# Kernel optimization log

Measured on AMD Instinct MI355X. Metric: run time of the kernel, lower is better.

Reference implementation:

```python
import jax, jax.numpy as jnp
import numpy as np
from jax import lax

DG = 8          # deformable groups
KH = KW = 3
K = KH * KW
PAD = 1


def conv3x3(x, w, b):
    # x: (B,C,H,W), w: (O,C,3,3) -> SAME conv, stride 1
    y = lax.conv_general_dilated(x, w, (1, 1), ((PAD, PAD), (PAD, PAD)),
                                 dimension_numbers=('NCHW', 'OIHW', 'NCHW'))
    return y + b[None, :, None, None]


def lrelu(x):
    return jnp.where(x >= 0, x, 0.1 * x)


def modulated_deform_conv(x, offset, mask, w, b):
    """DCNv2 semantics: stride=1, pad=1, dilation=1, groups=1.
    x: (B,C,H,W); offset: (B, 2*DG*K, H, W); mask: (B, DG*K, H, W) (already sigmoided);
    w: (O, C, 3, 3); b: (O,).
    Offset channel layout per CUDA kernel: (DG, K, 2[y,x]).
    """
    B, C, H, W = x.shape
    cg = C // DG
    off = offset.reshape(B, DG, K, 2, H, W)
    dy, dx = off[:, :, :, 0], off[:, :, :, 1]            # (B,DG,K,H,W)

    ky, kx = jnp.meshgrid(jnp.arange(KH), jnp.arange(KW), indexing='ij')
    ky = ky.reshape(K).astype(x.dtype)
    kx = kx.reshape(K).astype(x.dtype)
    base_y = jnp.arange(H, dtype=x.dtype)[None, :, None] - PAD + ky[:, None, None]  # (K,H,1)
    base_x = jnp.arange(W, dtype=x.dtype)[None, None, :] - PAD + kx[:, None, None]  # (K,1,W)
    py = dy + base_y                                     # (B,DG,K,H,W)
    px = dx + base_x

    y0 = jnp.floor(py)
    x0 = jnp.floor(px)
    wy = py - y0
    wx = px - x0
    y0i = y0.astype(jnp.int32)
    x0i = x0.astype(jnp.int32)

    xg = x.reshape(B, DG, cg, H * W)

    def gather(yi, xi):
        valid = ((yi >= 0) & (yi < H) & (xi >= 0) & (xi < W)).astype(x.dtype)
        idx = jnp.clip(yi, 0, H - 1) * W + jnp.clip(xi, 0, W - 1)   # (B,DG,K,H,W)
        idxf = idx.reshape(B, DG, 1, K * H * W)
        vals = jnp.take_along_axis(xg, jnp.broadcast_to(idxf, (B, DG, cg, K * H * W)), axis=3)
        return vals.reshape(B, DG, cg, K, H, W) * valid[:, :, None]

    samp = gather(y0i, x0i) * ((1 - wy) * (1 - wx))[:, :, None]
    samp = samp + gather(y0i, x0i + 1) * ((1 - wy) * wx)[:, :, None]
    samp = samp + gather(y0i + 1, x0i) * (wy * (1 - wx))[:, :, None]
    samp = samp + gather(y0i + 1, x0i + 1) * (wy * wx)[:, :, None]

    samp = samp * mask.reshape(B, DG, 1, K, H, W)        # modulated
    wr = w.reshape(w.shape[0], DG, cg, K)
    out = jnp.einsum('odck,bdckhw->bohw', wr, samp)
    return out + b[None, :, None, None]


def dcn_pack(x, feat, off_w, off_b, w, b):
    # conv_offset on `feat` -> (B, 3*DG*K, H, W); chunk into o1,o2,mask
    out = conv3x3(feat, off_w, off_b)
    o1, o2, m = jnp.split(out, 3, axis=1)
    offset = jnp.concatenate([o1, o2], axis=1)
    mask = jax.nn.sigmoid(m)
    return modulated_deform_conv(x, offset, mask, w, b)


def setup_inputs() -> dict:
    key = jax.random.key(0)
    ks = jax.random.split(key, 24)
    B, C, H, W = 4, 64, 192, 192
    nf = C

    def wconv(k, o, i, s=0.02):
        return jax.random.normal(k, (o, i, 3, 3), jnp.float32) * s

    inp = {
        'nbr_l1': jax.random.normal(ks[0], (B, C, H, W), jnp.float32),
        'ref_l1': jax.random.normal(ks[1], (B, C, H, W), jnp.float32),
        'oc1_w': wconv(ks[2], nf, 2 * nf), 'oc1_b': jnp.zeros((nf,), jnp.float32),
        'oc2_w': wconv(ks[3], nf, nf), 'oc2_b': jnp.zeros((nf,), jnp.float32),
        'dcn1_off_w': wconv(ks[4], 3 * DG * K, nf, 0.01), 'dcn1_off_b': jnp.zeros((3 * DG * K,), jnp.float32),
        'dcn1_w': wconv(ks[5], nf, nf), 'dcn1_b': jnp.zeros((nf,), jnp.float32),
        'fc_w': wconv(ks[6], nf, nf), 'fc_b': jnp.zeros((nf,), jnp.float32),
        'cas1_w': wconv(ks[7], nf, 2 * nf), 'cas1_b': jnp.zeros((nf,), jnp.float32),
        'cas2_w': wconv(ks[8], nf, nf), 'cas2_b': jnp.zeros((nf,), jnp.float32),
        'casd_off_w': wconv(ks[9], 3 * DG * K, nf, 0.01), 'casd_off_b': jnp.zeros((3 * DG * K,), jnp.float32),
        'casd_w': wconv(ks[10], nf, nf), 'casd_b': jnp.zeros((nf,), jnp.float32),
    }
    return inp


def reference(nbr_l1, ref_l1, oc1_w, oc1_b, oc2_w, oc2_b,
              dcn1_off_w, dcn1_off_b, dcn1_w, dcn1_b, fc_w, fc_b,
              cas1_w, cas1_b, cas2_w, cas2_b,
              casd_off_w, casd_off_b, casd_w, casd_b):
    offset = jnp.concatenate([nbr_l1, ref_l1], axis=1)
    offset = lrelu(conv3x3(offset, oc1_w, oc1_b))
    offset = lrelu(conv3x3(offset, oc2_w, oc2_b))
    feat = dcn_pack(nbr_l1, offset, dcn1_off_w, dcn1_off_b, dcn1_w, dcn1_b)
    feat = conv3x3(feat, fc_w, fc_b)                     # no activation (matches source)
    offset = jnp.concatenate([feat, ref_l1], axis=1)
    offset = lrelu(conv3x3(lrelu(conv3x3(offset, cas1_w, cas1_b)), cas2_w, cas2_b))
    feat = lrelu(dcn_pack(feat, offset, casd_off_w, casd_off_b, casd_w, casd_b))
    return feat
```

## Files before the change

kernel.cpp:

```cpp
#include <hip/hip_runtime.h>
#include <hip/hip_bf16.h>
#include <math.h>

typedef __hip_bfloat16 bf16;
typedef float  floatx16 __attribute__((ext_vector_type(16)));
typedef short  short8   __attribute__((ext_vector_type(8)));

#define Bn 4
#define NF 64
#define Hn 192
#define Wn 192
#define HWn (Hn*Wn)

#define WA_OC1  0
#define WA_OC2  73728
#define WA_FC   110592
#define WA_CAS1 147456
#define WA_CAS2 221184
#define WA_D1O  258048
#define WA_CDO  405504
#define WP_D1   552960
#define WP_CD   589824
#define B_OC1  0
#define B_OC2  64
#define B_FC   128
#define B_CAS1 192
#define B_CAS2 256
#define B_D1O  320
#define B_CDO  536
#define B_D1P  752
#define B_CDP  816
#define BIAS_OFF  1024
#define WPOOL_OFF 5120
#define BUF_OFF   1261568
#define FEAT_BYTES 18874368

#define WROWS 12
#define WCOLS 12
#define WSTR  72
#define SSTR2 152

__device__ __forceinline__ float b2f(bf16 v){ return __bfloat162float(v); }
__device__ __forceinline__ bf16  f2b(float v){ return __float2bfloat16(v); }
__device__ __forceinline__ float us2f(unsigned short u){ return __uint_as_float(((unsigned)u) << 16); }
__device__ __forceinline__ float ld(const void* p, size_t i, int f32){
    if (f32) return ((const float*)p)[i];
    return b2f(((const bf16*)p)[i]);
}

union B8 { uint2 u2[2]; uint4 u4; short8 s8; };
union V8 { uint4 u4; unsigned short us[8]; bf16 h[8]; };
union V4 { uint2 u2; bf16 h[4]; };

struct P20 { const void* p[20]; int n[20]; };

__global__ void detect_kernel(P20 a, int* __restrict__ flags){
    int t = threadIdx.x;
    if (t >= 20) return;
    const unsigned short* u = (const unsigned short*)a.p[t];
    int n = a.n[t]; if (n > 512) n = 512;
    int f32 = 0;
    for (int i = 0; i < n; ++i){
        float v = __uint_as_float(((unsigned)u[i]) << 16);
        if (!(fabsf(v) < 1e3f)) f32 = 1;
    }
    flags[t] = f32;
}

__global__ void prep_convA(const void* __restrict__ src, const int* __restrict__ flags,
                           int fi, bf16* __restrict__ dst, int Cin, int CoutReal, int OCB)
{
    int idx = blockIdx.x*256 + threadIdx.x;
    int KK = Cin >> 4;
    int total = OCB*9*KK*512;
    if (idx >= total) return;
    int j  = idx & 7;
    int ko = (idx>>3) & 1;
    int m  = (idx>>4) & 31;
    int rest = idx >> 9;
    int kk = rest % KK; rest /= KK;
    int tap = rest % 9;
    int ocb = rest / 9;
    int oc = ocb*32 + m;
    int ci = kk*16 + ko*8 + j;
    float v = 0.f;
    if (oc < CoutReal) v = ld(src, ((size_t)oc*Cin + ci)*9 + tap, flags[fi]);
    dst[idx] = f2b(v);
}

__global__ void prep_projA(const void* __restrict__ src, const int* __restrict__ flags,
                           int fi, bf16* __restrict__ dst)
{
    int idx = blockIdx.x*256 + threadIdx.x;
    if (idx >= 2*36*512) return;
    int j  = idx & 7;
    int ko = (idx>>3) & 1;
    int m  = (idx>>4) & 31;
    int rest = idx >> 9;
    int kk = rest % 36;
    int ocb = rest / 36;
    int oc = ocb*32 + m;
    int kp   = kk*16 + ko*8 + j;
    int slot = kp >> 3;
    int cg   = kp & 7;
    int dg   = slot / 9;
    int tap  = slot - dg*9;
    int k    = (dg*8 + cg)*9 + tap;
    dst[idx] = f2b(ld(src, (size_t)oc*576 + k, flags[fi]));
}

__global__ void prep_bias(P20 a, const int* __restrict__ flags, float* __restrict__ bp){
    int t = threadIdx.x;
    const int src[9] = {3,5,11,13,15,7,17,9,19};
    const int off[9] = {B_OC1,B_OC2,B_FC,B_CAS1,B_CAS2,B_D1O,B_CDO,B_D1P,B_CDP};
    const int sz[9]  = {64,64,64,64,64,216,216,64,64};
    for (int s = 0; s < 9; ++s)
        if (t < sz[s]) bp[off[s] + t] = ld(a.p[src[s]], t, flags[src[s]]);
}

__global__ __launch_bounds__(256)
void pack_x(const void* __restrict__ src, const int* __restrict__ flags, int fi,
            bf16* __restrict__ dst)
{
    __shared__ bf16 s[64*65];
    const int b    = blockIdx.y;
    const int pix0 = blockIdx.x * 64;
    const int t    = threadIdx.x;
    const int f    = (fi >= 0) ? flags[fi] : 0;

    const int px8 = (t & 7) * 8;
    const int ci0 = t >> 3;
#pragma unroll
    for (int it = 0; it < 2; ++it){
        int ci = ci0 + it*32;
        size_t g = ((size_t)b*NF + ci)*HWn + pix0 + px8;
        if (f){
            float4 a0 = *(const float4*)((const float*)src + g);
            float4 a1 = *(const float4*)((const float*)src + g + 4);
            bf16* sp = &s[ci*65 + px8];
            sp[0]=f2b(a0.x); sp[1]=f2b(a0.y); sp[2]=f2b(a0.z); sp[3]=f2b(a0.w);
            sp[4]=f2b(a1.x); sp[5]=f2b(a1.y); sp[6]=f2b(a1.z); sp[7]=f2b(a1.w);
        } else {
            V8 v; v.u4 = *(const uint4*)((const bf16*)src + g);
            bf16* sp = &s[ci*65 + px8];
#pragma unroll
            for (int j = 0; j < 8; ++j) sp[j] = v.h[j];
        }
    }
    __syncthreads();

    const int px  = t >> 2;
    const int ch0 = (t & 3) * 16;
    V8 o0, o1;
#pragma unroll
    for (int j = 0; j < 8; ++j){
        o0.h[j] = s[(ch0 + j)*65 + px];
        o1.h[j] = s[(ch0 + 8 + j)*65 + px];
    }
    bf16* dp = dst + ((size_t)b*HWn + pix0 + px)*64 + ch0;
    *(uint4*)(dp)     = o0.u4;
    *(uint4*)(dp + 8) = o1.u4;
}

__global__ __launch_bounds__(256)
void conv_mfma(const bf16* __restrict__ inA, const bf16* __restrict__ inB,
               const bf16* __restrict__ wA, const float* __restrict__ bias,
               bf16* __restrict__ out,
               int nOcb, int CoutReal, int OutChStore, int ACT)
{
    extern __shared__ __align__(16) char smem_raw[];
    bf16* s_in = (bf16*)smem_raw;

    const int CinT  = inB ? 128 : 64;
    const int ciPad = CinT + 4;
    const int b     = blockIdx.z;
    const int pix0  = blockIdx.x * 64;
    const int h     = pix0 / Wn;
    const int x0    = pix0 - h*Wn;
    const int tid   = threadIdx.x;

    for (int ky = 0; ky < 3; ++ky){
        const int y  = h - 1 + ky;
        const bool yv = (unsigned)y < (unsigned)Hn;
        const size_t rb = ((size_t)b*HWn + (size_t)y*Wn)*64;
        for (int e = tid; e < 528; e += 256){
            const int c = e >> 3, ch8 = e & 7;
            const int x = x0 - 1 + c;
            const bool v = yv && (unsigned)x < (unsigned)Wn;
            B8 va; va.u4 = make_uint4(0,0,0,0);
            if (v) va.u4 = *(const uint4*)(inA + rb + (size_t)x*64 + ch8*8);
            bf16* dp = &s_in[(ky*66 + c)*ciPad + ch8*8];
            *(uint2*)(dp)     = va.u2[0];
            *(uint2*)(dp + 4) = va.u2[1];
            if (inB){
                B8 vb; vb.u4 = make_uint4(0,0,0,0);
                if (v) vb.u4 = *(const uint4*)(inB + rb + (size_t)x*64 + ch8*8);
                bf16* dq = dp + 64;
                *(uint2*)(dq)     = vb.u2[0];
                *(uint2*)(dq + 4) = vb.u2[1];
            }
        }
    }
    __syncthreads();

    const int w    = tid >> 6;
    const int lane = tid & 63;
    const int m    = lane & 31;
    const int half = lane >> 5;
    const int och  = (w >> 1) * 32;
    const int pxh  = (w & 1) * 32;
    const int KK   = CinT >> 4;
    const int col0 = pxh + m;
    const int pxo  = pix0 + pxh + m;

    for (int ot = 0; ot < nOcb; ++ot){
        const int ocb = ot*2 + (w >> 1);
        floatx16 acc;
#pragma unroll
        for (int r = 0; r < 16; ++r) acc[r] = 0.f;

        const bf16* wAb = wA + ((size_t)ocb*9*KK)*512 + m*16 + half*8;
#pragma unroll
        for (int tap = 0; tap < 9; ++tap){
            const int ky = tap/3, kx = tap - (tap/3)*3;
            const bf16* srow = s_in + (ky*66 + col0 + kx)*ciPad + half*8;
            for (int kk = 0; kk < KK; ++kk){
                B8 ba; ba.u4 = *(const uint4*)(wAb + (size_t)(tap*KK + kk)*512);
                B8 bb;
                const bf16* sp = srow + kk*16;
                bb.u2[0] = *(const uint2*)(sp);
                bb.u2[1] = *(const uint2*)(sp + 4);
                acc = __builtin_amdgcn_mfma_f32_32x32x16_bf16(ba.s8, bb.s8, acc, 0, 0, 0);
            }
        }

        if (ACT == 2){
#pragma unroll
            for (int r = 0; r < 16; ++r){
                int row = (r & 3) + 8*(r >> 2) + 4*half;
                int oc  = ot*64 + och + row;
                if (oc < CoutReal){
                    float v = acc[r] + bias[oc];
                    if (oc >= 144) v = 1.f/(1.f + expf(-v));
                    out[((size_t)b*OutChStore + oc)*HWn + pxo] = f2b(v);
                }
            }
        } else {
            bf16* ob = out + ((size_t)b*HWn + pxo)*64 + och + 4*half;
#pragma unroll
            for (int q = 0; q < 4; ++q){
                V4 u;
#pragma unroll
                for (int j = 0; j < 4; ++j){
                    int oc = och + 4*half + 8*q + j;
                    float v = acc[q*4 + j] + bias[oc];
                    if (ACT == 1) v = (v >= 0.f) ? v : 0.1f*v;
                    u.h[j] = f2b(v);
                }
                *(uint2*)(ob + 8*q) = u.u2;
            }
        }
    }
}

__global__ __launch_bounds__(256, 2)
void dcn_mfma(const bf16* __restrict__ xi,
              const bf16* __restrict__ offs,
              const bf16* __restrict__ wP,
              const float* __restrict__ pbias,
              void* __restrict__ out, int outF32, int ACT)
{
    __shared__ __align__(16) bf16 s_win[WROWS*WCOLS*WSTR];
    __shared__ __align__(16) bf16 s_samp[64*SSTR2];

    const int b   = blockIdx.y;
    const int bx  = blockIdx.x;
    const int tx  = bx % (Wn/8);
    const int ty  = bx / (Wn/8);
    const int gx0 = tx*8, gy0 = ty*8;
    const int wx0 = gx0 - 2, wy0 = gy0 - 2;
    const int tid = threadIdx.x;

    const bf16* xb = xi + (size_t)b*HWn*64;

    for (int c = tid; c < WROWS*WCOLS*8; c += 256){
        int ch4 = c & 7;
        int pxi = c >> 3;
        int gy  = wy0 + pxi/WCOLS;
        int gx  = wx0 + pxi%WCOLS;
        uint4 v = {0u,0u,0u,0u};
        if ((unsigned)gy < (unsigned)Hn && (unsigned)gx < (unsigned)Wn)
            v = *(const uint4*)(xb + ((size_t)gy*Wn + gx)*64 + ch4*8);
        *(uint4*)&s_win[pxi*WSTR + ch4*8] = v;
    }

    const int px   = tid & 63;
    const int wq   = tid >> 6;
    const int pr   = px >> 3, pc = px & 7;
    const int gy   = gy0 + pr, gx = gx0 + pc;
    const int m    = px & 31;
    const int half = px >> 5;
    const int och  = (wq >> 1) * 32;
    const int pxh  = (wq & 1) * 32;

    const size_t obase = (size_t)b*216*HWn + (size_t)gy*Wn + gx;
    const uint4 z4 = {0u,0u,0u,0u};

    const bf16* wPb  = wP + ((size_t)(wq>>1)*36)*512 + m*16 + half*8;
    const bf16* srow = s_samp + (pxh + m)*SSTR2 + half*8;

    floatx16 acc;
#pragma unroll
    for (int r = 0; r < 16; ++r) acc[r] = 0.f;

    for (int pass = 0; pass < 4; ++pass){
        __syncthreads();

#pragma unroll
        for (int ii = 0; ii < 5; ++ii){
            int sl = wq + ii*4;
            if (sl < 18){
                int dgl = sl / 9;
                int tap = sl - dgl*9;
                int dg  = pass*2 + dgl;
                int ky  = tap / 3;
                int kx  = tap - ky*3;
                float dy = b2f(offs[obase + (size_t)(dg*18 + tap*2    )*HWn]);
                float dx = b2f(offs[obase + (size_t)(dg*18 + tap*2 + 1)*HWn]);
                float mk = b2f(offs[obase + (size_t)(144 + dg*9 + tap )*HWn]);
                float py  = dy + (float)(gy - 1 + ky);
                float pxx = dx + (float)(gx - 1 + kx);
                float y0f = floorf(py), x0f = floorf(pxx);
                int   y0  = (int)y0f,   xi0 = (int)x0f;
                float wy  = py - y0f,   wx  = pxx - x0f;
                float w00 = (1.f-wy)*(1.f-wx)*mk, w01 = (1.f-wy)*wx*mk;
                float w10 = wy*(1.f-wx)*mk,       w11 = wy*wx*mk;
                int ly = y0 - wy0, lx = xi0 - wx0;

                auto fetch = [&](int ly_, int lx_, int y_, int x_) -> uint4 {
                    if ((unsigned)ly_ < (unsigned)WROWS && (unsigned)lx_ < (unsigned)WCOLS)
                        return *(const uint4*)&s_win[(ly_*WCOLS + lx_)*WSTR + dg*8];
                    if ((unsigned)y_ < (unsigned)Hn && (unsigned)x_ < (unsigned)Wn)
                        return *(const uint4*)(xb + ((size_t)y_*Wn + x_)*64 + dg*8);
                    return z4;
                };
                V8 c00, c01, c10, c11, o;
                c00.u4 = fetch(ly,   lx,   y0,   xi0  );
                c01.u4 = fetch(ly,   lx+1, y0,   xi0+1);
                c10.u4 = fetch(ly+1, lx,   y0+1, xi0  );
                c11.u4 = fetch(ly+1, lx+1, y0+1, xi0+1);
#pragma unroll
                for (int j = 0; j < 8; ++j){
                    float v = w00*us2f(c00.us[j]) + w01*us2f(c01.us[j])
                            + w10*us2f(c10.us[j]) + w11*us2f(c11.us[j]);
                    o.h[j] = f2b(v);
                }
                *(uint4*)&s_samp[px*SSTR2 + sl*8] = o.u4;
            }
        }
        __syncthreads();

#pragma unroll
        for (int kk = 0; kk < 9; ++kk){
            B8 ba; ba.u4 = *(const uint4*)(wPb + (size_t)(pass*9 + kk)*512);
            B8 bb; bb.u4 = *(const uint4*)(srow + kk*16);
            acc = __builtin_amdgcn_mfma_f32_32x32x16_bf16(ba.s8, bb.s8, acc, 0, 0, 0);
        }
    }

    const int opx = pxh + m;
    const int pxo = (gy0 + (opx >> 3))*Wn + gx0 + (opx & 7);
    if (outF32){
#pragma unroll
        for (int r = 0; r < 16; ++r){
            int row = (r & 3) + 8*(r >> 2) + 4*half;
            int oc  = och + row;
            float v = acc[r] + pbias[oc];
            if (ACT) v = (v >= 0.f) ? v : 0.1f*v;
            ((float*)out)[((size_t)b*NF + oc)*HWn + pxo] = v;
        }
    } else {
        bf16* ob = (bf16*)out + ((size_t)b*HWn + pxo)*64 + och + 4*half;
#pragma unroll
        for (int q = 0; q < 4; ++q){
            V4 u;
#pragma unroll
            for (int j = 0; j < 4; ++j){
                int oc = och + 4*half + 8*q + j;
                float v = acc[q*4 + j] + pbias[oc];
                if (ACT) v = (v >= 0.f) ? v : 0.1f*v;
                u.h[j] = f2b(v);
            }
            *(uint2*)(ob + 8*q) = u.u2;
        }
    }
}

extern "C" void kernel_launch(void* const* d_in, const int* in_sizes, int n_in,
                              void* d_out, int out_size, void* d_ws, size_t ws_size,
                              hipStream_t stream)
{
    enum { I_NBR=0, I_REF=1, I_OC1W=2, I_OC2W=4, I_D1OW=6, I_D1W=8, I_FCW=10,
           I_C1W=12, I_C2W=14, I_CDOW=16, I_CDW=18 };

    int*   flags = (int*)d_ws;
    float* bp    = (float*)((char*)d_ws + BIAS_OFF);
    bf16*  wp    = (bf16*) ((char*)d_ws + WPOOL_OFF);
    bf16*  t1    = (bf16*) ((char*)d_ws + BUF_OFF);
    bf16*  f1    = (bf16*) ((char*)d_ws + BUF_OFF + FEAT_BYTES);
    bf16*  offs  = (bf16*) ((char*)d_ws + BUF_OFF + 2*(size_t)FEAT_BYTES);
    bf16*  t0    = (bf16*) d_out;
    bf16*  nbr_i = (bf16*)((char*)d_out + FEAT_BYTES);
    bf16*  refA  = offs;
    bf16*  refB  = nbr_i;

    P20 a;
    for (int i = 0; i < 20; ++i){ a.p[i] = d_in[i]; a.n[i] = in_sizes[i]; }

    detect_kernel<<<1, 64, 0, stream>>>(a, flags);
    prep_bias<<<1, 256, 0, stream>>>(a, flags, bp);
    prep_convA<<<288, 256, 0, stream>>>(d_in[I_OC1W], flags, I_OC1W, wp+WA_OC1, 128, 64, 2);
    prep_convA<<<144, 256, 0, stream>>>(d_in[I_OC2W], flags, I_OC2W, wp+WA_OC2,  64, 64, 2);
    prep_convA<<<144, 256, 0, stream>>>(d_in[I_FCW],  flags, I_FCW,  wp+WA_FC,   64, 64, 2);
    prep_convA<<<288, 256, 0, stream>>>(d_in[I_C1W],  flags, I_C1W,  wp+WA_CAS1,128, 64, 2);
    prep_convA<<<144, 256, 0, stream>>>(d_in[I_C2W],  flags, I_C2W,  wp+WA_CAS2, 64, 64, 2);
    prep_convA<<<576, 256, 0, stream>>>(d_in[I_D1OW], flags, I_D1OW, wp+WA_D1O,  64, 216, 8);
    prep_convA<<<576, 256, 0, stream>>>(d_in[I_CDOW], flags, I_CDOW, wp+WA_CDO,  64, 216, 8);
    prep_projA<<<144, 256, 0, stream>>>(d_in[I_D1W],  flags, I_D1W,  wp+WP_D1);
    prep_projA<<<144, 256, 0, stream>>>(d_in[I_CDW],  flags, I_CDW,  wp+WP_CD);

    dim3 blk(256,1,1);
    const int smem64  = 3*66*68*2;
    const int smem128 = 3*66*132*2;
    dim3 gC (576, 1, Bn);
    dim3 gD (576, Bn, 1);
    dim3 gP (576, Bn, 1);

    pack_x<<<gP, blk, 0, stream>>>(d_in[I_NBR], flags, I_NBR, nbr_i);
    pack_x<<<gP, blk, 0, stream>>>(d_in[I_REF], flags, I_REF, refA);
    conv_mfma<<<gC, blk, smem128, stream>>>(nbr_i, refA, wp+WA_OC1, bp+B_OC1,
        t0, 1, 64, 64, 1);
    conv_mfma<<<gC, blk, smem64, stream>>>(t0, nullptr, wp+WA_OC2, bp+B_OC2,
        t1, 1, 64, 64, 1);
    conv_mfma<<<gC, blk, smem64, stream>>>(t1, nullptr, wp+WA_D1O, bp+B_D1O,
        offs, 4, 216, 216, 2);
    dcn_mfma<<<gD, blk, 0, stream>>>(nbr_i, offs, wp+WP_D1, bp+B_D1P,
        t1, 0, 0);
    pack_x<<<gP, blk, 0, stream>>>(d_in[I_REF], flags, I_REF, refB);
    conv_mfma<<<gC, blk, smem64, stream>>>(t1, nullptr, wp+WA_FC, bp+B_FC,
        f1, 1, 64, 64, 0);
    conv_mfma<<<gC, blk, smem128, stream>>>(f1, refB, wp+WA_CAS1, bp+B_CAS1,
        t0, 1, 64, 64, 1);
    conv_mfma<<<gC, blk, smem64, stream>>>(t0, nullptr, wp+WA_CAS2, bp+B_CAS2,
        t1, 1, 64, 64, 1);
    conv_mfma<<<gC, blk, smem64, stream>>>(t1, nullptr, wp+WA_CDO, bp+B_CDO,
        offs, 4, 216, 216, 2);
    dcn_mfma<<<gD, blk, 0, stream>>>(f1, offs, wp+WP_CD, bp+B_CDP,
        d_out, 1, 1);
}
```

Baseline: 893.7 us.

## Tile conv over two output rows with double-buffered weights and merged prep kernels

The conv kernel now computes a 2-row by 64-pixel tile per block, with each wave issuing two MFMAs per weight fragment. This halves the weight loads per output and shares the input halo rows. Weight fragments are prefetched through a two-slot register ring, and channel counts become template parameters so the loops are fully unrolled. The weight and bias preparation launches are merged into two kernels to cut launch overhead, at the cost of higher register pressure and more shared memory per block.

```diff
diff --git a/kernel.cpp b/kernel.cpp
--- a/kernel.cpp
+++ b/kernel.cpp
@@ -54,68 +54,69 @@
 
 struct P20 { const void* p[20]; int n[20]; };
 
-__global__ void detect_kernel(P20 a, int* __restrict__ flags){
+__global__ void detect_bias(P20 a, int* __restrict__ flags, float* __restrict__ bp){
+    __shared__ int sf[20];
     int t = threadIdx.x;
-    if (t >= 20) return;
-    const unsigned short* u = (const unsigned short*)a.p[t];
-    int n = a.n[t]; if (n > 512) n = 512;
-    int f32 = 0;
-    for (int i = 0; i < n; ++i){
-        float v = __uint_as_float(((unsigned)u[i]) << 16);
-        if (!(fabsf(v) < 1e3f)) f32 = 1;
-    }
-    flags[t] = f32;
-}
-
-__global__ void prep_convA(const void* __restrict__ src, const int* __restrict__ flags,
-                           int fi, bf16* __restrict__ dst, int Cin, int CoutReal, int OCB)
-{
-    int idx = blockIdx.x*256 + threadIdx.x;
-    int KK = Cin >> 4;
-    int total = OCB*9*KK*512;
-    if (idx >= total) return;
-    int j  = idx & 7;
-    int ko = (idx>>3) & 1;
-    int m  = (idx>>4) & 31;
-    int rest = idx >> 9;
-    int kk = rest % KK; rest /= KK;
-    int tap = rest % 9;
-    int ocb = rest / 9;
-    int oc = ocb*32 + m;
-    int ci = kk*16 + ko*8 + j;
-    float v = 0.f;
-    if (oc < CoutReal) v = ld(src, ((size_t)oc*Cin + ci)*9 + tap, flags[fi]);
-    dst[idx] = f2b(v);
-}
-
-__global__ void prep_projA(const void* __restrict__ src, const int* __restrict__ flags,
-                           int fi, bf16* __restrict__ dst)
-{
-    int idx = blockIdx.x*256 + threadIdx.x;
-    if (idx >= 2*36*512) return;
-    int j  = idx & 7;
-    int ko = (idx>>3) & 1;
-    int m  = (idx>>4) & 31;
-    int rest = idx >> 9;
-    int kk = rest % 36;
-    int ocb = rest / 36;
-    int oc = ocb*32 + m;
-    int kp   = kk*16 + ko*8 + j;
-    int slot = kp >> 3;
-    int cg   = kp & 7;
-    int dg   = slot / 9;
-    int tap  = slot - dg*9;
-    int k    = (dg*8 + cg)*9 + tap;
-    dst[idx] = f2b(ld(src, (size_t)oc*576 + k, flags[fi]));
-}
-
-__global__ void prep_bias(P20 a, const int* __restrict__ flags, float* __restrict__ bp){
-    int t = threadIdx.x;
+    if (t < 20){
+        const unsigned short* u = (const unsigned short*)a.p[t];
+        int n = a.n[t]; if (n > 512) n = 512;
+        int f32 = 0;
+        for (int i = 0; i < n; ++i){
+            float v = __uint_as_float(((unsigned)u[i]) << 16);
+            if (!(fabsf(v) < 1e3f)) f32 = 1;
+        }
+        sf[t] = f32; flags[t] = f32;
+    }
+    __syncthreads();
     const int src[9] = {3,5,11,13,15,7,17,9,19};
     const int off[9] = {B_OC1,B_OC2,B_FC,B_CAS1,B_CAS2,B_D1O,B_CDO,B_D1P,B_CDP};
     const int sz[9]  = {64,64,64,64,64,216,216,64,64};
     for (int s = 0; s < 9; ++s)
-        if (t < sz[s]) bp[off[s] + t] = ld(a.p[src[s]], t, flags[src[s]]);
+        if (t < sz[s]) bp[off[s] + t] = ld(a.p[src[s]], t, sf[src[s]]);
+}
+
+__global__ void prep_weights(P20 a, const int* __restrict__ flags, bf16* __restrict__ wp)
+{
+    const int srcI[9] = {2,4,10,12,14,6,16,8,18};
+    const int dstO[9] = {WA_OC1,WA_OC2,WA_FC,WA_CAS1,WA_CAS2,WA_D1O,WA_CDO,WP_D1,WP_CD};
+    const int cinA[9] = {128,64,64,128,64,64,64,0,0};
+    const int coutA[9]= {64,64,64,64,64,216,216,0,0};
+    const int nblk[9] = {288,144,144,288,144,576,576,144,144};
+
+    int bx = blockIdx.x;
+    int j = 0, base = 0;
+    while (j < 8 && bx >= base + nblk[j]){ base += nblk[j]; ++j; }
+    int idx = (bx - base)*256 + threadIdx.x;
+    const void* src = a.p[srcI[j]];
+    const int f = flags[srcI[j]];
+    bf16* dst = wp + dstO[j];
+
+    int jj = idx & 7;
+    int ko = (idx>>3) & 1;
+    int mm = (idx>>4) & 31;
+    int rest = idx >> 9;
+    if (cinA[j]){
+        int KK = cinA[j] >> 4;
+        int kk = rest % KK; rest /= KK;
+        int tap = rest % 9;
+        int ocb = rest / 9;
+        int oc = ocb*32 + mm;
+        int ci = kk*16 + ko*8 + jj;
+        float v = 0.f;
+        if (oc < coutA[j]) v = ld(src, ((size_t)oc*cinA[j] + ci)*9 + tap, f);
+        dst[idx] = f2b(v);
+    } else {
+        int kk = rest % 36;
+        int ocb = rest / 36;
+        int oc = ocb*32 + mm;
+        int kp   = kk*16 + ko*8 + jj;
+        int slot = kp >> 3;
+        int cg   = kp & 7;
+        int dg   = slot / 9;
+        int tap  = slot - dg*9;
+        int k    = (dg*8 + cg)*9 + tap;
+        dst[idx] = f2b(ld(src, (size_t)oc*576 + k, f));
+    }
 }
 
 __global__ __launch_bounds__(256)
@@ -162,43 +163,41 @@
     *(uint4*)(dp + 8) = o1.u4;
 }
 
-__global__ __launch_bounds__(256)
+template<int KK, int NOCB>
+__global__ __launch_bounds__(256, 2)
 void conv_mfma(const bf16* __restrict__ inA, const bf16* __restrict__ inB,
                const bf16* __restrict__ wA, const float* __restrict__ bias,
-               bf16* __restrict__ out,
-               int nOcb, int CoutReal, int OutChStore, int ACT)
+               bf16* __restrict__ out, int ACT)
 {
+    constexpr int CinT  = KK*16;
+    constexpr int ciPad = CinT + 4;
+    constexpr int CH8   = CinT/8;
+    constexpr int CSH   = (KK==4)?3:4;
     extern __shared__ __align__(16) char smem_raw[];
     bf16* s_in = (bf16*)smem_raw;
 
-    const int CinT  = inB ? 128 : 64;
-    const int ciPad = CinT + 4;
-    const int b     = blockIdx.z;
-    const int pix0  = blockIdx.x * 64;
-    const int h     = pix0 / Wn;
-    const int x0    = pix0 - h*Wn;
-    const int tid   = threadIdx.x;
-
-    for (int ky = 0; ky < 3; ++ky){
-        const int y  = h - 1 + ky;
+    const int b  = blockIdx.z;
+    const int bx = blockIdx.x;
+    const int ty = bx/3, tx = bx - ty*3;
+    const int h0 = ty*2, x0 = tx*64;
+    const int tid = threadIdx.x;
+
+    for (int r = 0; r < 4; ++r){
+        const int y = h0 - 1 + r;
         const bool yv = (unsigned)y < (unsigned)Hn;
         const size_t rb = ((size_t)b*HWn + (size_t)y*Wn)*64;
-        for (int e = tid; e < 528; e += 256){
-            const int c = e >> 3, ch8 = e & 7;
+        for (int e = tid; e < 66*CH8; e += 256){
+            const int c   = e >> CSH;
+            const int ch8 = e & (CH8-1);
             const int x = x0 - 1 + c;
-            const bool v = yv && (unsigned)x < (unsigned)Wn;
-            B8 va; va.u4 = make_uint4(0,0,0,0);
-            if (v) va.u4 = *(const uint4*)(inA + rb + (size_t)x*64 + ch8*8);
-            bf16* dp = &s_in[(ky*66 + c)*ciPad + ch8*8];
-            *(uint2*)(dp)     = va.u2[0];
-            *(uint2*)(dp + 4) = va.u2[1];
-            if (inB){
-                B8 vb; vb.u4 = make_uint4(0,0,0,0);
-                if (v) vb.u4 = *(const uint4*)(inB + rb + (size_t)x*64 + ch8*8);
-                bf16* dq = dp + 64;
-                *(uint2*)(dq)     = vb.u2[0];
-                *(uint2*)(dq + 4) = vb.u2[1];
-            }
+            B8 v; v.u4 = make_uint4(0,0,0,0);
+            if (yv && (unsigned)x < (unsigned)Wn){
+                if (KK==8 && ch8 >= 8) v.u4 = *(const uint4*)(inB + rb + (size_t)x*64 + (ch8-8)*8);
+                else                   v.u4 = *(const uint4*)(inA + rb + (size_t)x*64 + ch8*8);
+            }
+            bf16* dp = &s_in[(size_t)(r*66 + c)*ciPad + ch8*8];
+            *(uint2*)(dp)     = v.u2[0];
+            *(uint2*)(dp + 4) = v.u2[1];
         }
     }
     __syncthreads();
@@ -208,56 +207,80 @@
     const int m    = lane & 31;
     const int half = lane >> 5;
     const int och  = (w >> 1) * 32;
-    const int pxh  = (w & 1) * 32;
-    const int KK   = CinT >> 4;
-    const int col0 = pxh + m;
-    const int pxo  = pix0 + pxh + m;
-
-    for (int ot = 0; ot < nOcb; ++ot){
+    const int rw   = (w & 1);
+    const int gpx0 = (h0 + rw)*Wn + x0;
+
+#pragma unroll
+    for (int ot = 0; ot < NOCB; ++ot){
         const int ocb = ot*2 + (w >> 1);
-        floatx16 acc;
-#pragma unroll
-        for (int r = 0; r < 16; ++r) acc[r] = 0.f;
-
-        const bf16* wAb = wA + ((size_t)ocb*9*KK)*512 + m*16 + half*8;
+        const bf16* wb = wA + ((size_t)ocb*9*KK)*512 + m*16 + half*8;
+
+        floatx16 a0, a1;
+#pragma unroll
+        for (int r = 0; r < 16; ++r){ a0[r] = 0.f; a1[r] = 0.f; }
+
+        B8 ring[2][4];
+#pragma unroll
+        for (int i = 0; i < 4; ++i) ring[0][i].u4 = *(const uint4*)(wb + (size_t)i*512);
+
+        constexpr int NCH = 9*KK/4;
 #pragma unroll
         for (int tap = 0; tap < 9; ++tap){
-            const int ky = tap/3, kx = tap - (tap/3)*3;
-            const bf16* srow = s_in + (ky*66 + col0 + kx)*ciPad + half*8;
-            for (int kk = 0; kk < KK; ++kk){
-                B8 ba; ba.u4 = *(const uint4*)(wAb + (size_t)(tap*KK + kk)*512);
-                B8 bb;
-                const bf16* sp = srow + kk*16;
-                bb.u2[0] = *(const uint2*)(sp);
-                bb.u2[1] = *(const uint2*)(sp + 4);
-                acc = __builtin_amdgcn_mfma_f32_32x32x16_bf16(ba.s8, bb.s8, acc, 0, 0, 0);
+            const int ky = tap/3, kx = tap - 3*(tap/3);
+            const bf16* s0 = s_in + (size_t)((ky+rw)*66 + kx + m)*ciPad + half*8;
+#pragma unroll
+            for (int hh = 0; hh < KK/4; ++hh){
+                const int cidx = tap*(KK/4) + hh;
+                const int cur = cidx & 1, nxt = cur ^ 1;
+                if (cidx + 1 < NCH){
+#pragma unroll
+                    for (int i = 0; i < 4; ++i)
+                        ring[nxt][i].u4 = *(const uint4*)(wb + (size_t)((cidx+1)*4 + i)*512);
+                }
+#pragma unroll
+                for (int i = 0; i < 4; ++i){
+                    const bf16* p0 = s0 + hh*64 + i*16;
+                    const bf16* p1 = p0 + 32*ciPad;
+                    B8 b0, b1;
+                    b0.u2[0] = *(const uint2*)(p0); b0.u2[1] = *(const uint2*)(p0+4);
+                    b1.u2[0] = *(const uint2*)(p1); b1.u2[1] = *(const uint2*)(p1+4);
+                    a0 = __builtin_amdgcn_mfma_f32_32x32x16_bf16(ring[cur][i].s8, b0.s8, a0, 0,0,0);
+                    a1 = __builtin_amdgcn_mfma_f32_32x32x16_bf16(ring[cur][i].s8, b1.s8, a1, 0,0,0);
+                }
             }
         }
 
         if (ACT == 2){
 #pragma unroll
-            for (int r = 0; r < 16; ++r){
-                int row = (r & 3) + 8*(r >> 2) + 4*half;
-                int oc  = ot*64 + och + row;
-                if (oc < CoutReal){
-                    float v = acc[r] + bias[oc];
-                    if (oc >= 144) v = 1.f/(1.f + expf(-v));
-                    out[((size_t)b*OutChStore + oc)*HWn + pxo] = f2b(v);
+            for (int s = 0; s < 2; ++s){
+                const int px = gpx0 + s*32 + m;
+#pragma unroll
+                for (int r = 0; r < 16; ++r){
+                    int row = (r & 3) + 8*(r >> 2) + 4*half;
+                    int oc  = ot*64 + och + row;
+                    if (oc < 216){
+                        float v = (s ? a1[r] : a0[r]) + bias[oc];
+                        if (oc >= 144) v = 1.f/(1.f + __expf(-v));
+                        out[((size_t)b*216 + oc)*HWn + px] = f2b(v);
+                    }
                 }
             }
         } else {
-            bf16* ob = out + ((size_t)b*HWn + pxo)*64 + och + 4*half;
-#pragma unroll
-            for (int q = 0; q < 4; ++q){
-                V4 u;
-#pragma unroll
-                for (int j = 0; j < 4; ++j){
-                    int oc = och + 4*half + 8*q + j;
-                    float v = acc[q*4 + j] + bias[oc];
-                    if (ACT == 1) v = (v >= 0.f) ? v : 0.1f*v;
-                    u.h[j] = f2b(v);
+#pragma unroll
+            for (int s = 0; s < 2; ++s){
+                const int px = gpx0 + s*32 + m;
+                bf16* ob = out + ((size_t)b*HWn + px)*64 + och + 4*half;
+#pragma unroll
+                for (int q = 0; q < 4; ++q){
+                    V4 u;
+#pragma unroll
+                    for (int j = 0; j < 4; ++j){
+                        float v = (s ? a1[q*4+j] : a0[q*4+j]) + bias[och + 4*half + 8*q + j];
+                        if (ACT == 1) v = (v >= 0.f) ? v : 0.1f*v;
+                        u.h[j] = f2b(v);
+                    }
+                    *(uint2*)(ob + 8*q) = u.u2;
                 }
-                *(uint2*)(ob + 8*q) = u.u2;
             }
         }
     }
@@ -400,8 +423,7 @@
                               void* d_out, int out_size, void* d_ws, size_t ws_size,
                               hipStream_t stream)
 {
-    enum { I_NBR=0, I_REF=1, I_OC1W=2, I_OC2W=4, I_D1OW=6, I_D1W=8, I_FCW=10,
-           I_C1W=12, I_C2W=14, I_CDOW=16, I_CDW=18 };
+    enum { I_NBR=0, I_REF=1 };
 
     int*   flags = (int*)d_ws;
     float* bp    = (float*)((char*)d_ws + BIAS_OFF);
@@ -417,44 +439,26 @@
     P20 a;
     for (int i = 0; i < 20; ++i){ a.p[i] = d_in[i]; a.n[i] = in_sizes[i]; }
 
-    detect_kernel<<<1, 64, 0, stream>>>(a, flags);
-    prep_bias<<<1, 256, 0, stream>>>(a, flags, bp);
-    prep_convA<<<288, 256, 0, stream>>>(d_in[I_OC1W], flags, I_OC1W, wp+WA_OC1, 128, 64, 2);
-    prep_convA<<<144, 256, 0, stream>>>(d_in[I_OC2W], flags, I_OC2W, wp+WA_OC2,  64, 64, 2);
-    prep_convA<<<144, 256, 0, stream>>>(d_in[I_FCW],  flags, I_FCW,  wp+WA_FC,   64, 64, 2);
-    prep_convA<<<288, 256, 0, stream>>>(d_in[I_C1W],  flags, I_C1W,  wp+WA_CAS1,128, 64, 2);
-    prep_convA<<<144, 256, 0, stream>>>(d_in[I_C2W],  flags, I_C2W,  wp+WA_CAS2, 64, 64, 2);
-    prep_convA<<<576, 256, 0, stream>>>(d_in[I_D1OW], flags, I_D1OW, wp+WA_D1O,  64, 216, 8);
-    prep_convA<<<576, 256, 0, stream>>>(d_in[I_CDOW], flags, I_CDOW, wp+WA_CDO,  64, 216, 8);
-    prep_projA<<<144, 256, 0, stream>>>(d_in[I_D1W],  flags, I_D1W,  wp+WP_D1);
-    prep_projA<<<144, 256, 0, stream>>>(d_in[I_CDW],  flags, I_CDW,  wp+WP_CD);
+    detect_bias<<<1, 256, 0, stream>>>(a, flags, bp);
+    prep_weights<<<2448, 256, 0, stream>>>(a, flags, wp);
 
     dim3 blk(256,1,1);
-    const int smem64  = 3*66*68*2;
-    const int smem128 = 3*66*132*2;
-    dim3 gC (576, 1, Bn);
+    const int smem64  = 4*66*68*2;
+    const int smem128 = 4*66*132*2;
+    dim3 gC (288, 1, Bn);
     dim3 gD (576, Bn, 1);
     dim3 gP (576, Bn, 1);
 
     pack_x<<<gP, blk, 0, stream>>>(d_in[I_NBR], flags, I_NBR, nbr_i);
     pack_x<<<gP, blk, 0, stream>>>(d_in[I_REF], flags, I_REF, refA);
-    conv_mfma<<<gC, blk, smem128, stream>>>(nbr_i, refA, wp+WA_OC1, bp+B_OC1,
-        t0, 1, 64, 64, 1);
-    conv_mfma<<<gC, blk, smem64, stream>>>(t0, nullptr, wp+WA_OC2, bp+B_OC2,
-        t1, 1, 64, 64, 1);
-    conv_mfma<<<gC, blk, smem64, stream>>>(t1, nullptr, wp+WA_D1O, bp+B_D1O,
-        offs, 4, 216, 216, 2);
-    dcn_mfma<<<gD, blk, 0, stream>>>(nbr_i, offs, wp+WP_D1, bp+B_D1P,
-        t1, 0, 0);
+    conv_mfma<8,1><<<gC, blk, smem128, stream>>>(nbr_i, refA, wp+WA_OC1, bp+B_OC1, t0, 1);
+    conv_mfma<4,1><<<gC, blk, smem64, stream>>>(t1==t1?t0:t0, nullptr, wp+WA_OC2, bp+B_OC2, t1, 1);
+    conv_mfma<4,4><<<gC, blk, smem64, stream>>>(t1, nullptr, wp+WA_D1O, bp+B_D1O, offs, 2);
+    dcn_mfma<<<gD, blk, 0, stream>>>(nbr_i, offs, wp+WP_D1, bp+B_D1P, t1, 0, 0);
     pack_x<<<gP, blk, 0, stream>>>(d_in[I_REF], flags, I_REF, refB);
-    conv_mfma<<<gC, blk, smem64, stream>>>(t1, nullptr, wp+WA_FC, bp+B_FC,
-        f1, 1, 64, 64, 0);
-    conv_mfma<<<gC, blk, smem128, stream>>>(f1, refB, wp+WA_CAS1, bp+B_CAS1,
-        t0, 1, 64, 64, 1);
-    conv_mfma<<<gC, blk, smem64, stream>>>(t0, nullptr, wp+WA_CAS2, bp+B_CAS2,
-        t1, 1, 64, 64, 1);
-    conv_mfma<<<gC, blk, smem64, stream>>>(t1, nullptr, wp+WA_CDO, bp+B_CDO,
-        offs, 4, 216, 216, 2);
-    dcn_mfma<<<gD, blk, 0, stream>>>(f1, offs, wp+WP_CD, bp+B_CDP,
-        d_out, 1, 1);
-}
+    conv_mfma<4,1><<<gC, blk, smem64, stream>>>(t1, nullptr, wp+WA_FC, bp+B_FC, f1, 0);
+    conv_mfma<8,1><<<gC, blk, smem128, stream>>>(f1, refB, wp+WA_CAS1, bp+B_CAS1, t0, 1);
+    conv_mfma<4,1><<<gC, blk, smem64, stream>>>(t0, nullptr, wp+WA_CAS2, bp+B_CAS2, t1, 1);
+    conv_mfma<4,4><<<gC, blk, smem64, stream>>>(t1, nullptr, wp+WA_CDO, bp+B_CDO, offs, 2);
+    dcn_mfma<<<gD, blk, 0, stream>>>(f1, offs, wp+WP_CD, bp+B_CDP, d_out, 1, 1);
+}
```

Result: faster. 858.6 us (-3.9%).
